# Performance work log

Hardware: AMD Instinct MI355X
Metric: run time of the kernel (lower is better)

Reference implementation:

```python
import jax, jax.numpy as jnp
import numpy as np

B, H, W, C = 4, 128, 128, 256
APL = 3  # anchors per location


def setup_inputs() -> dict:
    key = jax.random.key(0)
    ks = jax.random.split(key, 4)
    inputs = jax.random.normal(ks[0], (B, H, W, C), dtype=jnp.float32)
    # he_normal-ish scaled weights
    w_shared = jax.random.normal(ks[1], (3, 3, C, 512), dtype=jnp.float32) * (2.0 / (3 * 3 * C)) ** 0.5
    b_shared = jnp.zeros((512,), dtype=jnp.float32)
    w_cls = jax.random.normal(ks[2], (1, 1, 512, 2 * APL), dtype=jnp.float32) * (2.0 / 512) ** 0.5
    b_cls = jnp.zeros((2 * APL,), dtype=jnp.float32)
    w_delta = jax.random.normal(ks[3], (1, 1, 512, 4 * APL), dtype=jnp.float32) * (2.0 / 512) ** 0.5
    b_delta = jnp.zeros((4 * APL,), dtype=jnp.float32)
    return {"inputs": inputs, "w_shared": w_shared, "b_shared": b_shared,
            "w_cls": w_cls, "b_cls": b_cls, "w_delta": w_delta, "b_delta": b_delta}


def reference(inputs, w_shared, b_shared, w_cls, b_cls, w_delta, b_delta):
    # rpn_conv_shared: 3x3 SAME conv -> ReLU
    shared = jax.lax.conv_general_dilated(
        inputs, w_shared, window_strides=(1, 1), padding='SAME',
        dimension_numbers=('NHWC', 'HWIO', 'NHWC')) + b_shared
    shared = jax.nn.relu(shared)
    b = inputs.shape[0]
    # 1x1 convs are just per-pixel matmuls
    cls = jnp.einsum('bhwc,co->bhwo', shared, w_cls[0, 0]) + b_cls
    rpn_class_logits = cls.reshape(b, -1, 2)  # [B, num_anchors, 2]
    rpn_probs = jax.nn.softmax(rpn_class_logits, axis=-1)
    dlt = jnp.einsum('bhwc,co->bhwo', shared, w_delta[0, 0]) + b_delta
    rpn_deltas = dlt.reshape(b, -1, 4)  # [B, num_anchors, 4]
    return (rpn_class_logits, rpn_probs, rpn_deltas)
```

## Files before the change

kernel.cpp:

```cpp
#include <hip/hip_runtime.h>
#include <stdint.h>

#define BATCH 4
#define HH 128
#define WW 128
#define CIN 256
#define CO 512
#define HP 130
#define NPIX (BATCH*HH*WW)
#define LOGITS_N (NPIX*6)
#define DELTA_BASE (2*LOGITS_N)

typedef short bf16x8 __attribute__((ext_vector_type(8)));
typedef unsigned short u16x8 __attribute__((ext_vector_type(8)));
typedef float f32x4 __attribute__((ext_vector_type(4)));
typedef unsigned int u32;

__device__ __forceinline__ unsigned short f2bf(float f) {
    union { float f; unsigned int u; } v; v.f = f;
    return (unsigned short)((v.u + 0x7FFFu + ((v.u >> 16) & 1u)) >> 16);
}

__device__ __forceinline__ void gload16(const unsigned short* g, char* l) {
    __builtin_amdgcn_global_load_lds(
        (const __attribute__((address_space(1))) u32*)g,
        (__attribute__((address_space(3))) u32*)l, 16, 0, 0);
}

__global__ __launch_bounds__(256) void k_pad_convert(const float* __restrict__ in,
                                                     unsigned short* __restrict__ out) {
    size_t q = (size_t)blockIdx.x*256 + threadIdx.x;
    if (q >= (size_t)BATCH*HP*HP*64) return;
    int c4 = ((int)q & 63) * 4;
    int pix = (int)(q >> 6);
    int xx = pix % HP; int t = pix / HP; int yy = t % HP; int b = t / HP;
    ushort4 r = {0, 0, 0, 0};
    if (yy >= 1 && yy <= HH && xx >= 1 && xx <= WW) {
        const float4 v = *(const float4*)(in + (((size_t)(b*HH) + (yy-1))*WW + (xx-1))*CIN + c4);
        r.x = f2bf(v.x); r.y = f2bf(v.y); r.z = f2bf(v.z); r.w = f2bf(v.w);
    }
    *(ushort4*)(out + (size_t)pix*CIN + c4) = r;
}

__global__ __launch_bounds__(256) void k_wt_convert(const float* __restrict__ w,
                                                    unsigned short* __restrict__ wt) {
    int n = blockIdx.x % CO; int tap = blockIdx.x / CO;
    int c = threadIdx.x;
    wt[((size_t)tap*CO + n)*CIN + c] = f2bf(w[((size_t)tap*CIN + c)*CO + n]);
}

__global__ __launch_bounds__(512, 2) void k_main8(
    const unsigned short* __restrict__ in_p,
    const unsigned short* __restrict__ wt,
    const float* __restrict__ b_sh,
    const float* __restrict__ w_cls,
    const float* __restrict__ w_dlt,
    float* __restrict__ part)
{
    extern __shared__ char LDS[];

    const int tid  = threadIdx.x;
    const int lane = tid & 63, wave = tid >> 6;
    const int l15  = lane & 15, l4 = lane >> 4;
    const int wm   = wave >> 2, wn = wave & 3;

    const int bid   = ((blockIdx.x & 7) << 6) + (blockIdx.x >> 3);
    const int ntile = bid & 1, mtile = bid >> 1;
    const int n0 = ntile << 8;
    const int b  = mtile >> 6;
    const int y0 = (mtile & 63) * 2;

    const int rl0 = tid >> 3, pc0 = tid & 7;
    const int kc0 = pc0 ^ (rl0 & 7);
    const int off = rl0*256 + kc0*8;
    const int t16 = tid*16;

    int base_a[2], base_b[2];
    #pragma unroll
    for (int kk = 0; kk < 2; kk++) {
        int swz = ((kk*32 + l4*8)*2) ^ ((l15 & 7) << 4);
        base_a[kk] = (wm*128 + l15)*128 + swz;
        base_b[kk] = 32768 + (wn*64 + l15)*128 + swz;
    }

    f32x4 acc[8][4];
    const f32x4 zz = {0.f, 0.f, 0.f, 0.f};
    #pragma unroll
    for (int mi = 0; mi < 8; mi++)
        #pragma unroll
        for (int ni = 0; ni < 4; ni++) acc[mi][ni] = zz;

    {
        const unsigned short* gB0 = wt + (size_t)n0*256;
        const unsigned short* gA0 = in_p + ((size_t)(b*HP + y0))*HP*256;
        char* Ad0 = LDS; char* Bd0 = LDS + 32768;
        gload16(gB0 + off,          Bd0 + t16);
        gload16(gB0 + 16384 + off,  Bd0 + 8192 + t16);
        gload16(gB0 + 32768 + off,  Bd0 + 16384 + t16);
        gload16(gB0 + 49152 + off,  Bd0 + 24576 + t16);
        gload16(gA0 + off,          Ad0 + t16);
        gload16(gA0 + 33280 + off,  Ad0 + 16384 + t16);
        gload16(gA0 + 16384 + off,  Ad0 + 8192 + t16);
        gload16(gA0 + 49664 + off,  Ad0 + 24576 + t16);
    }
    asm volatile("s_waitcnt vmcnt(2)" ::: "memory");
    __builtin_amdgcn_sched_barrier(0);
    __builtin_amdgcn_s_barrier();
    __builtin_amdgcn_sched_barrier(0);

#define MFMA16(Q)                                                            \
    __builtin_amdgcn_s_setprio(1);                                           \
    _Pragma("unroll")                                                        \
    for (int kk = 0; kk < 2; kk++)                                           \
        _Pragma("unroll")                                                    \
        for (int mm = 0; mm < 2; mm++)                                       \
            _Pragma("unroll")                                                \
            for (int ni = 0; ni < 4; ni++)                                   \
                acc[2*(Q)+mm][ni] = __builtin_amdgcn_mfma_f32_16x16x32_bf16( \
                    a_[mm][kk], breg[ni][kk], acc[2*(Q)+mm][ni], 0, 0, 0);   \
    __builtin_amdgcn_s_setprio(0);

#define BAR       __builtin_amdgcn_s_barrier(); __builtin_amdgcn_sched_barrier(0);
#define LOAD_AQ(Q)                                                           \
    bf16x8 a_[2][2];                                                         \
    _Pragma("unroll")                                                        \
    for (int kk = 0; kk < 2; kk++) {                                         \
        a_[0][kk] = *(const bf16x8*)(bufc + base_a[kk] + (2*(Q))*2048);      \
        a_[1][kk] = *(const bf16x8*)(bufc + base_a[kk] + (2*(Q)+1)*2048);    \
    }

    for (int s = 0; s < 36; ++s) {
        const int s1 = s + 1;
        const int tap1 = s1 >> 2, kq1 = s1 & 3;
        const int dy1 = (tap1*11) >> 5, dx1 = tap1 - dy1*3;
        const unsigned short* gA = in_p + ((size_t)((b*HP + y0 + dy1)*HP + dx1))*256 + kq1*64;
        const unsigned short* gB = wt + ((size_t)(tap1*512 + n0))*256 + kq1*64;
        const int cur = s & 1;
        const char* bufc = LDS + (cur << 16);
        char* Ad = LDS + ((cur ^ 1) << 16);
        char* Bd = Ad + 32768;
        const bool more = (s < 35);

        bf16x8 breg[4][2];

        {
            bf16x8 a_[2][2];
            #pragma unroll
            for (int kk = 0; kk < 2; kk++) {
                a_[0][kk]  = *(const bf16x8*)(bufc + base_a[kk]);
                a_[1][kk]  = *(const bf16x8*)(bufc + base_a[kk] + 2048);
                breg[0][kk] = *(const bf16x8*)(bufc + base_b[kk]);
                breg[1][kk] = *(const bf16x8*)(bufc + base_b[kk] + 2048);
                breg[2][kk] = *(const bf16x8*)(bufc + base_b[kk] + 4096);
                breg[3][kk] = *(const bf16x8*)(bufc + base_b[kk] + 6144);
            }
            if (more) { gload16(gB + off,         Bd + t16);
                        gload16(gB + 16384 + off, Bd + 8192 + t16); }
            BAR
            MFMA16(0)
            BAR
        }
        {
            LOAD_AQ(1)
            if (more) { gload16(gB + 32768 + off, Bd + 16384 + t16);
                        gload16(gB + 49152 + off, Bd + 24576 + t16); }
            BAR
            MFMA16(1)
            if (more) { asm volatile("s_waitcnt vmcnt(4)" ::: "memory"); }
            else      { asm volatile("s_waitcnt vmcnt(0)" ::: "memory"); }
            __builtin_amdgcn_sched_barrier(0);
            BAR
        }
        {
            LOAD_AQ(2)
            if (more) { gload16(gA + off,         Ad + t16);
                        gload16(gA + 33280 + off, Ad + 16384 + t16); }
            BAR
            MFMA16(2)
            BAR
        }
        {
            LOAD_AQ(3)
            if (more) { gload16(gA + 16384 + off, Ad + 8192 + t16);
                        gload16(gA + 49664 + off, Ad + 24576 + t16); }
            BAR
            MFMA16(3)
            if (more) { asm volatile("s_waitcnt vmcnt(2)" ::: "memory");
                        __builtin_amdgcn_sched_barrier(0); }
            BAR
        }
    }
#undef MFMA16
#undef BAR
#undef LOAD_AQ

    float* shf = (float*)LDS;
    float* sW  = (float*)(LDS + 66560);
    for (int j = tid; j < 256*18; j += 512) {
        int c = j / 18, o = j - c*18;
        sW[c*20 + o] = (o < 6) ? w_cls[(size_t)(n0 + c)*6 + o]
                               : w_dlt[(size_t)(n0 + c)*12 + (o - 6)];
    }
    float bsh[4];
    #pragma unroll
    for (int ni = 0; ni < 4; ni++) bsh[ni] = b_sh[n0 + wn*64 + ni*16 + l15];

    float a18[18];
    #pragma unroll
    for (int o = 0; o < 18; o++) a18[o] = 0.f;
    const int rr = tid & 255, chalf = tid >> 8;
    __syncthreads();

    for (int p = 0; p < 4; ++p) {
        if (wn == p) {
            #pragma unroll
            for (int mi = 0; mi < 8; mi++)
                #pragma unroll
                for (int ni = 0; ni < 4; ni++) {
                    int colL = ni*16 + l15;
                    int row0 = wm*128 + mi*16 + l4*4;
                    f32x4 v = acc[mi][ni];
                    f32x4 sv;
                    #pragma unroll
                    for (int r = 0; r < 4; r++) sv[r] = fmaxf(v[r] + bsh[ni], 0.f);
                    *(f32x4*)(shf + colL*260 + row0) = sv;
                }
        }
        __syncthreads();
        #pragma unroll 4
        for (int i = 0; i < 32; i++) {
            int c = chalf*32 + i;
            float v = shf[c*260 + rr];
            const float* wrow = sW + (p*64 + c)*20;
            #pragma unroll
            for (int o = 0; o < 18; o++) a18[o] += v * wrow[o];
        }
        __syncthreads();
    }

    if (chalf == 1) {
        #pragma unroll
        for (int o = 0; o < 18; o++) shf[rr*18 + o] = a18[o];
    }
    __syncthreads();
    if (chalf == 0) {
        float* dst = part + ((size_t)ntile*NPIX + (size_t)mtile*256 + rr)*18;
        #pragma unroll
        for (int o = 0; o < 18; o++) dst[o] = a18[o] + shf[rr*18 + o];
    }
}

__global__ __launch_bounds__(256) void k_finalize_ws(const float* __restrict__ part,
                                                     float* __restrict__ out,
                                                     const float* __restrict__ b_cls,
                                                     const float* __restrict__ b_dlt) {
    int pix = blockIdx.x*256 + threadIdx.x;
    if (pix >= NPIX) return;
    float s[18];
    #pragma unroll
    for (int o = 0; o < 18; o++)
        s[o] = part[(size_t)pix*18 + o] + part[((size_t)NPIX + pix)*18 + o];
    float* lo = out + (size_t)pix*6;
    float* pr = out + (size_t)LOGITS_N + (size_t)pix*6;
    float* dl = out + (size_t)DELTA_BASE + (size_t)pix*12;
    #pragma unroll
    for (int a = 0; a < 3; a++) {
        float l0 = s[a*2]   + b_cls[a*2];
        float l1 = s[a*2+1] + b_cls[a*2+1];
        lo[a*2] = l0; lo[a*2+1] = l1;
        float m = fmaxf(l0, l1);
        float e0 = __expf(l0 - m), e1 = __expf(l1 - m);
        float inv = 1.f / (e0 + e1);
        pr[a*2] = e0*inv; pr[a*2+1] = e1*inv;
    }
    #pragma unroll
    for (int o = 0; o < 12; o++) dl[o] = s[6 + o] + b_dlt[o];
}

__global__ __launch_bounds__(256) void k_main_fb(
    const float* __restrict__ in_f, const float* __restrict__ w_f,
    const float* __restrict__ b_sh, const float* __restrict__ w_cls,
    const float* __restrict__ w_dlt, float* __restrict__ out)
{
    __shared__ float smemf[11008];
    char* smem  = (char*)smemf;
    char* smemB = smem + 16384;
    const int tid = threadIdx.x;
    const int lane = tid & 63, wave = tid >> 6;
    const int l15 = lane & 15, l4 = lane >> 4;
    const int wr = wave >> 1, wc = wave & 1;
    int bid = ((blockIdx.x & 7) << 8) + (blockIdx.x >> 3);
    const int ntile = bid & 3, mtile = bid >> 2;
    const int n0 = ntile << 7;
    const int b = mtile >> 7, y = mtile & 127;
    int aoff[4][2], boff[4][2];
    #pragma unroll
    for (int mi = 0; mi < 4; mi++) {
        int rowA = wr*64 + mi*16 + l15;
        int rowB = wc*64 + mi*16 + l15;
        #pragma unroll
        for (int kk = 0; kk < 2; kk++) {
            int kb = (kk*32 + l4*8) * 2;
            aoff[mi][kk] = rowA*128 + (kb ^ ((rowA & 7) << 4));
            boff[mi][kk] = rowB*128 + (kb ^ ((rowB & 7) << 4));
        }
    }
    f32x4 acc[4][4];
    const f32x4 zz = {0.f, 0.f, 0.f, 0.f};
    #pragma unroll
    for (int mi = 0; mi < 4; mi++)
        #pragma unroll
        for (int ni = 0; ni < 4; ni++) acc[mi][ni] = zz;
    for (int s = 0; s < 36; s++) {
        int tap = s >> 2, kq = s & 3;
        int dy = tap / 3, dx = tap - dy*3;
        const int c0 = kq * 64;
        const int yy = y + dy - 1;
        const bool yok = (yy >= 0) && (yy < HH);
        #pragma unroll
        for (int i = 0; i < 4; i++) {
            int ci = i*256 + tid;
            int row = ci >> 3, pc = ci & 7;
            int kc = pc ^ (row & 7);
            int xx = row + dx - 1;
            u16x8 a;
            if (yok && xx >= 0 && xx < WW) {
                const float* sp = in_f + (((size_t)(b*HH) + yy)*WW + xx)*CIN + c0 + kc*8;
                #pragma unroll
                for (int j = 0; j < 8; j++) a[j] = (short)f2bf(sp[j]);
            } else {
                #pragma unroll
                for (int j = 0; j < 8; j++) a[j] = 0;
            }
            *(u16x8*)(smem + ci*16) = a;
            const float* wsrc = w_f + ((size_t)(tap*CIN + c0 + kc*8))*CO + n0 + row;
            u16x8 bb;
            #pragma unroll
            for (int j = 0; j < 8; j++) bb[j] = (short)f2bf(wsrc[(size_t)j*CO]);
            *(u16x8*)(smemB + ci*16) = bb;
        }
        __syncthreads();
        #pragma unroll
        for (int kk = 0; kk < 2; kk++) {
            bf16x8 av[4], bv[4];
            #pragma unroll
            for (int mi = 0; mi < 4; mi++) av[mi] = *(const bf16x8*)(smem  + aoff[mi][kk]);
            #pragma unroll
            for (int ni = 0; ni < 4; ni++) bv[ni] = *(const bf16x8*)(smemB + boff[ni][kk]);
            #pragma unroll
            for (int mi = 0; mi < 4; mi++)
                #pragma unroll
                for (int ni = 0; ni < 4; ni++)
                    acc[mi][ni] = __builtin_amdgcn_mfma_f32_16x16x32_bf16(
                        av[mi], bv[ni], acc[mi][ni], 0, 0, 0);
        }
        __syncthreads();
    }
    float* shf = smemf;
    float* sW  = smemf + 8448;
    for (int j = tid; j < 128*18; j += 256) {
        int c = j / 18, o = j - c*18;
        sW[c*20 + o] = (o < 6) ? w_cls[(size_t)(n0 + c)*6 + o]
                               : w_dlt[(size_t)(n0 + c)*12 + (o - 6)];
    }
    float bsh[4];
    #pragma unroll
    for (int ni = 0; ni < 4; ni++) bsh[ni] = b_sh[n0 + wc*64 + ni*16 + l15];
    float a18[18];
    #pragma unroll
    for (int o = 0; o < 18; o++) a18[o] = 0.f;
    const int rr = tid & 127, chalf = tid >> 7;
    #pragma unroll
    for (int pass = 0; pass < 2; pass++) {
        if (wc == pass) {
            #pragma unroll
            for (int mi = 0; mi < 4; mi++)
                #pragma unroll
                for (int ni = 0; ni < 4; ni++) {
                    int colL = ni*16 + l15;
                    int row0 = wr*64 + mi*16 + l4*4;
                    f32x4 v = acc[mi][ni];
                    f32x4 sv;
                    #pragma unroll
                    for (int r = 0; r < 4; r++) sv[r] = fmaxf(v[r] + bsh[ni], 0.f);
                    *(f32x4*)(shf + colL*132 + row0) = sv;
                }
        }
        __syncthreads();
        #pragma unroll 4
        for (int i = 0; i < 32; i++) {
            int c = chalf*32 + i;
            float v = shf[c*132 + rr];
            const float* wrow = sW + (pass*64 + c)*20;
            #pragma unroll
            for (int o = 0; o < 18; o++) a18[o] += v * wrow[o];
        }
        __syncthreads();
    }
    const int pixel = mtile*128 + rr;
    float* lo = out + (size_t)pixel*6;
    float* dl = out + DELTA_BASE + (size_t)pixel*12;
    #pragma unroll
    for (int o = 0; o < 6; o++)  atomicAdd(lo + o, a18[o]);
    #pragma unroll
    for (int o = 0; o < 12; o++) atomicAdd(dl + o, a18[6 + o]);
}

__global__ __launch_bounds__(256) void k_finalize(float* __restrict__ out,
                                                  const float* __restrict__ b_cls,
                                                  const float* __restrict__ b_dlt) {
    int pix = blockIdx.x*256 + threadIdx.x;
    if (pix >= NPIX) return;
    float* lo = out + (size_t)pix*6;
    float* pr = out + (size_t)LOGITS_N + (size_t)pix*6;
    float* dl = out + (size_t)DELTA_BASE + (size_t)pix*12;
    #pragma unroll
    for (int a = 0; a < 3; a++) {
        float l0 = lo[a*2]   + b_cls[a*2];
        float l1 = lo[a*2+1] + b_cls[a*2+1];
        lo[a*2] = l0; lo[a*2+1] = l1;
        float m = fmaxf(l0, l1);
        float e0 = __expf(l0 - m), e1 = __expf(l1 - m);
        float inv = 1.f / (e0 + e1);
        pr[a*2] = e0*inv; pr[a*2+1] = e1*inv;
    }
    #pragma unroll
    for (int o = 0; o < 12; o++) dl[o] += b_dlt[o];
}

extern "C" void kernel_launch(void* const* d_in, const int* in_sizes, int n_in,
                              void* d_out, int out_size, void* d_ws, size_t ws_size,
                              hipStream_t stream) {
    const float* in    = (const float*)d_in[0];
    const float* w_sh  = (const float*)d_in[1];
    const float* b_sh  = (const float*)d_in[2];
    const float* w_cls = (const float*)d_in[3];
    const float* b_cls = (const float*)d_in[4];
    const float* w_dlt = (const float*)d_in[5];
    const float* b_dlt = (const float*)d_in[6];
    float* out = (float*)d_out;

    const size_t in_p_elems = (size_t)BATCH*HP*HP*CIN;
    const size_t wt_elems   = (size_t)9*CO*CIN;
    const size_t part_elems = (size_t)2*NPIX*18;
    const size_t need = (in_p_elems + wt_elems)*2 + part_elems*4;

    if (ws_size >= need) {
        unsigned short* in_p = (unsigned short*)d_ws;
        unsigned short* wt   = in_p + in_p_elems;
        float* part = (float*)(wt + wt_elems);
        hipFuncSetAttribute((const void*)k_main8,
                            hipFuncAttributeMaxDynamicSharedMemorySize, 131072);
        int padq = (int)(((size_t)BATCH*HP*HP*64 + 255)/256);
        k_pad_convert<<<padq, 256, 0, stream>>>(in, in_p);
        k_wt_convert<<<9*CO, 256, 0, stream>>>(w_sh, wt);
        k_main8<<<512, 512, 131072, stream>>>(in_p, wt, b_sh, w_cls, w_dlt, part);
        k_finalize_ws<<<(NPIX + 255)/256, 256, 0, stream>>>(part, out, b_cls, b_dlt);
    } else {
        hipMemsetAsync(d_out, 0, (size_t)out_size * sizeof(float), stream);
        k_main_fb<<<2048, 256, 0, stream>>>(in, w_sh, b_sh, w_cls, w_dlt, out);
        k_finalize<<<(NPIX + 255)/256, 256, 0, stream>>>(out, b_cls, b_dlt);
    }
}
```

Measured before the change: 200.0 us.

## Issue all next-stage loads upfront and use one barrier per K-stage

The main conv GEMM loop is restructured: all eight global-to-LDS loads for the next stage are issued at the start of each iteration. The four MFMA quarters then run back to back, with a single workgroup barrier at the end of the stage instead of eight barriers interleaved with the loads. The aim is to cut barrier stalls and let the waves run MFMAs more independently. The risk is that the mid-stage vmcnt wait has no following barrier, so LDS data written by other waves' async loads may not be visible before LOAD_AQ(2/3) reads it.

```diff
diff --git a/kernel.cpp b/kernel.cpp
--- a/kernel.cpp
+++ b/kernel.cpp
@@ -108,7 +108,7 @@
     __builtin_amdgcn_s_barrier();
     __builtin_amdgcn_sched_barrier(0);
 
-#define MFMA16(Q)                                                            \
+#define MFMA_Q(Q)                                                            \
     __builtin_amdgcn_s_setprio(1);                                           \
     _Pragma("unroll")                                                        \
     for (int kk = 0; kk < 2; kk++)                                           \
@@ -117,16 +117,14 @@
             _Pragma("unroll")                                                \
             for (int ni = 0; ni < 4; ni++)                                   \
                 acc[2*(Q)+mm][ni] = __builtin_amdgcn_mfma_f32_16x16x32_bf16( \
-                    a_[mm][kk], breg[ni][kk], acc[2*(Q)+mm][ni], 0, 0, 0);   \
+                    aq[mm][kk], breg[ni][kk], acc[2*(Q)+mm][ni], 0, 0, 0);   \
     __builtin_amdgcn_s_setprio(0);
 
-#define BAR       __builtin_amdgcn_s_barrier(); __builtin_amdgcn_sched_barrier(0);
 #define LOAD_AQ(Q)                                                           \
-    bf16x8 a_[2][2];                                                         \
     _Pragma("unroll")                                                        \
     for (int kk = 0; kk < 2; kk++) {                                         \
-        a_[0][kk] = *(const bf16x8*)(bufc + base_a[kk] + (2*(Q))*2048);      \
-        a_[1][kk] = *(const bf16x8*)(bufc + base_a[kk] + (2*(Q)+1)*2048);    \
+        aq[0][kk] = *(const bf16x8*)(bufc + base_a[kk] + (2*(Q))*2048);      \
+        aq[1][kk] = *(const bf16x8*)(bufc + base_a[kk] + (2*(Q)+1)*2048);    \
     }
 
     for (int s = 0; s < 36; ++s) {
@@ -141,57 +139,44 @@
         char* Bd = Ad + 32768;
         const bool more = (s < 35);
 
+        if (more) {
+            gload16(gB + off,          Bd + t16);
+            gload16(gB + 16384 + off,  Bd + 8192 + t16);
+            gload16(gB + 32768 + off,  Bd + 16384 + t16);
+            gload16(gB + 49152 + off,  Bd + 24576 + t16);
+            gload16(gA + off,          Ad + t16);
+            gload16(gA + 33280 + off,  Ad + 16384 + t16);
+            gload16(gA + 16384 + off,  Ad + 8192 + t16);
+            gload16(gA + 49664 + off,  Ad + 24576 + t16);
+        }
+
         bf16x8 breg[4][2];
-
-        {
-            bf16x8 a_[2][2];
-            #pragma unroll
-            for (int kk = 0; kk < 2; kk++) {
-                a_[0][kk]  = *(const bf16x8*)(bufc + base_a[kk]);
-                a_[1][kk]  = *(const bf16x8*)(bufc + base_a[kk] + 2048);
-                breg[0][kk] = *(const bf16x8*)(bufc + base_b[kk]);
-                breg[1][kk] = *(const bf16x8*)(bufc + base_b[kk] + 2048);
-                breg[2][kk] = *(const bf16x8*)(bufc + base_b[kk] + 4096);
-                breg[3][kk] = *(const bf16x8*)(bufc + base_b[kk] + 6144);
-            }
-            if (more) { gload16(gB + off,         Bd + t16);
-                        gload16(gB + 16384 + off, Bd + 8192 + t16); }
-            BAR
-            MFMA16(0)
-            BAR
-        }
-        {
-            LOAD_AQ(1)
-            if (more) { gload16(gB + 32768 + off, Bd + 16384 + t16);
-                        gload16(gB + 49152 + off, Bd + 24576 + t16); }
-            BAR
-            MFMA16(1)
-            if (more) { asm volatile("s_waitcnt vmcnt(4)" ::: "memory"); }
-            else      { asm volatile("s_waitcnt vmcnt(0)" ::: "memory"); }
-            __builtin_amdgcn_sched_barrier(0);
-            BAR
-        }
-        {
-            LOAD_AQ(2)
-            if (more) { gload16(gA + off,         Ad + t16);
-                        gload16(gA + 33280 + off, Ad + 16384 + t16); }
-            BAR
-            MFMA16(2)
-            BAR
-        }
-        {
-            LOAD_AQ(3)
-            if (more) { gload16(gA + 16384 + off, Ad + 8192 + t16);
-                        gload16(gA + 49664 + off, Ad + 24576 + t16); }
-            BAR
-            MFMA16(3)
-            if (more) { asm volatile("s_waitcnt vmcnt(2)" ::: "memory");
-                        __builtin_amdgcn_sched_barrier(0); }
-            BAR
-        }
-    }
-#undef MFMA16
-#undef BAR
+        #pragma unroll
+        for (int kk = 0; kk < 2; kk++) {
+            breg[0][kk] = *(const bf16x8*)(bufc + base_b[kk]);
+            breg[1][kk] = *(const bf16x8*)(bufc + base_b[kk] + 2048);
+            breg[2][kk] = *(const bf16x8*)(bufc + base_b[kk] + 4096);
+            breg[3][kk] = *(const bf16x8*)(bufc + base_b[kk] + 6144);
+        }
+        bf16x8 aq[2][2];
+        LOAD_AQ(0)
+        MFMA_Q(0)
+        LOAD_AQ(1)
+        MFMA_Q(1)
+        if (more) { asm volatile("s_waitcnt vmcnt(8)" ::: "memory"); }
+        else      { asm volatile("s_waitcnt vmcnt(0)" ::: "memory"); }
+        __builtin_amdgcn_sched_barrier(0);
+        LOAD_AQ(2)
+        MFMA_Q(2)
+        LOAD_AQ(3)
+        MFMA_Q(3)
+
+        if (more) { asm volatile("s_waitcnt vmcnt(2)" ::: "memory"); }
+        __builtin_amdgcn_sched_barrier(0);
+        __builtin_amdgcn_s_barrier();
+        __builtin_amdgcn_sched_barrier(0);
+    }
+#undef MFMA_Q
 #undef LOAD_AQ
 
     float* shf = (float*)LDS;
```

Result: no change. 198.0 us (-1.0%).
